# Performance work log

Hardware: AMD Instinct MI355X
Metric: run time of the kernel (lower is better)

## Reference

```python
import jax, jax.numpy as jnp
import numpy as np

N = 20000      # nodes
L = 64         # seq_length
E = 64         # emb_size
V = 30000      # vocab_size
HG = 128       # gnn_hidden_size
HT = 128       # text_hidden_size
NE = 640000    # edges
EPS = 1e-12


def _normalize(x):
    # F.normalize(x, p=2, dim=1) on [N, E, L]
    n = jnp.sqrt(jnp.sum(x * x, axis=1, keepdims=True))
    return x / jnp.maximum(n, EPS)


def gcn_conv(x, W, b, src_idx, dst_idx, n_nodes):
    # PyG GCNConv: add self-loops, symmetric normalization D^-1/2 (A+I) D^-1/2 (X W) + b
    h = x @ W                                            # [N, out]
    deg = jnp.zeros((n_nodes,), h.dtype).at[dst_idx].add(1.0) + 1.0  # incl. self-loop
    dinv = jax.lax.rsqrt(deg)
    norm = dinv[src_idx] * dinv[dst_idx]                 # [NE]
    msg = h[src_idx] * norm[:, None]                     # gather + scale
    out = jnp.zeros_like(h).at[dst_idx].add(msg)         # scatter-add to targets
    out = out + h * (dinv * dinv)[:, None]               # self-loop term
    return out + b


def setup_inputs() -> dict:
    key = jax.random.key(0)
    ks = jax.random.split(key, 12)
    rn = lambda k, shape: jax.random.normal(k, shape, jnp.float32) * 0.02
    return {
        "src": jax.random.randint(ks[0], (N, L), 0, V),
        "seg": jax.random.randint(ks[1], (N, L), 0, 3),
        "edge_index": jax.random.randint(ks[2], (2, NE), 0, N),
        "src_emb": rn(ks[3], (V, E)),
        "seg_emb": rn(ks[4], (3, E)),
        "w": jnp.ones((L,), jnp.float32),
        "Wq1": rn(ks[5], (E, HT)), "bq1": jnp.zeros((HT,), jnp.float32),
        "Wq2": rn(ks[6], (HT, E)), "bq2": jnp.zeros((E,), jnp.float32),
        "Wg1": rn(ks[7], (E, HG)), "bg1": jnp.zeros((HG,), jnp.float32),
        "Wg2": rn(ks[8], (HG, E)), "bg2": jnp.zeros((E,), jnp.float32),
        "Wl": rn(ks[9], (E, E)),   "bl": jnp.zeros((E,), jnp.float32),
    }


def reference(src, seg, edge_index, src_emb, seg_emb, w, Wq1, bq1, Wq2, bq2,
              Wg1, bg1, Wg2, bg2, Wl, bl):
    # --- LiteratureEmbedding ---
    se = src_emb[src]                 # [N, L, E]
    ge = seg_emb[seg]                 # [N, L, E]
    sv = se.reshape(-1, E, L)         # raw view (matches torch .view, not transpose)
    gv = ge.reshape(-1, E, L)
    f = (_normalize(w * sv) + _normalize(gv)).sum(-1)   # [N, E]
    # --- query MLP ---
    x = jax.nn.relu(f @ Wq1 + bq1) @ Wq2 + bq2
    # --- two GCN layers ---
    si, di = edge_index[0], edge_index[1]
    x = jax.nn.relu(gcn_conv(x, Wg1, bg1, si, di, N))
    x = jax.nn.relu(gcn_conv(x, Wg2, bg2, si, di, N))
    # --- output linear (dropout is identity in eval) ---
    return x @ Wl + bl
```

## Files before the change

### kernel.cpp

```cpp
#include <hip/hip_runtime.h>

#if defined(__has_builtin)
#if __has_builtin(__builtin_amdgcn_readlane)
#define READLANE(v, l) __builtin_amdgcn_readlane((v), (l))
#else
#define READLANE(v, l) __shfl((v), (l))
#endif
#else
#define READLANE(v, l) __shfl((v), (l))
#endif
__device__ __forceinline__ float readlane_f(float v, int l) {
    return __uint_as_float(READLANE(__float_as_uint(v), l));
}

__device__ __forceinline__ unsigned short f2bf(float x) {
    unsigned u = __float_as_uint(x);
    u += 0x7FFFu + ((u >> 16) & 1u);
    return (unsigned short)(u >> 16);
}

#define CAPLOG 8

__global__ __launch_bounds__(256) void zero_k(int* __restrict__ p,
                                              unsigned* __restrict__ Cz,
                                              unsigned* __restrict__ Az, int n) {
    int i = blockIdx.x * 256 + threadIdx.x;
    if (i < n) p[i] = 0;
    if (i < 32) { Cz[i] = 0u; Az[i] = 0u; }
}

__global__ __launch_bounds__(256) void fillb_k(const int* __restrict__ si,
                                               const int* __restrict__ di,
                                               int* __restrict__ cursor,
                                               int* __restrict__ edge_off, int ne) {
    int i = blockIdx.x * 256 + threadIdx.x;
    if (i < ne) {
        int d = di[i];
        int pos = atomicAdd(cursor + d, 1);
        edge_off[((long)d << CAPLOG) + pos] = si[i] << 7;
    }
}

__device__ __forceinline__ float4 csr_gather4_bf(const char* __restrict__ hb,
                                                 const int* __restrict__ eo,
                                                 int dn, int j, int zoff)
{
    const int grp = j >> 4;
    const int col = (j & 15) << 3;
    float4 a0 = make_float4(0.f, 0.f, 0.f, 0.f);
    float4 a1 = a0, a2 = a0, a3 = a0;
#define ACC(d, a)                                                        \
    { a.x += __uint_as_float((d).x << 16);                               \
      a.y += __uint_as_float((d).x & 0xFFFF0000u);                       \
      a.z += __uint_as_float((d).y << 16);                               \
      a.w += __uint_as_float((d).y & 0xFFFF0000u); }
    for (int e = 0; e < dn; e += 64) {
        const int cnt = min(dn - e, 64);
        const int eoff = (e + j < dn) ? eo[e + j] : zoff;
        int m = 0;
        for (; m + 16 <= cnt; m += 16) {
            int o0 = __shfl(eoff, m + grp);
            int o1 = __shfl(eoff, m + 4 + grp);
            int o2 = __shfl(eoff, m + 8 + grp);
            int o3 = __shfl(eoff, m + 12 + grp);
            uint2 d0 = *(const uint2*)(hb + (o0 + col));
            uint2 d1 = *(const uint2*)(hb + (o1 + col));
            uint2 d2 = *(const uint2*)(hb + (o2 + col));
            uint2 d3 = *(const uint2*)(hb + (o3 + col));
            ACC(d0, a0); ACC(d1, a1); ACC(d2, a2); ACC(d3, a3);
        }
        for (; m < cnt; m += 4) {
            int o = __shfl(eoff, m + grp);
            uint2 d = *(const uint2*)(hb + (o + col));
            ACC(d, a0);
        }
    }
#undef ACC
    a0.x += a1.x + a2.x + a3.x;
    a0.y += a1.y + a2.y + a3.y;
    a0.z += a1.z + a2.z + a3.z;
    a0.w += a1.w + a2.w + a3.w;
    a0.x += __shfl_xor(a0.x, 16); a0.x += __shfl_xor(a0.x, 32);
    a0.y += __shfl_xor(a0.y, 16); a0.y += __shfl_xor(a0.y, 32);
    a0.z += __shfl_xor(a0.z, 16); a0.z += __shfl_xor(a0.z, 32);
    a0.w += __shfl_xor(a0.w, 16); a0.w += __shfl_xor(a0.w, 32);
    return a0;
}

__device__ __forceinline__ float4 bf_row4(const char* hb, long rowoff, int col) {
    uint2 d = *(const uint2*)(hb + rowoff + col);
    float4 v;
    v.x = __uint_as_float(d.x << 16);
    v.y = __uint_as_float(d.x & 0xFFFF0000u);
    v.z = __uint_as_float(d.y << 16);
    v.w = __uint_as_float(d.y & 0xFFFF0000u);
    return v;
}

__global__ __launch_bounds__(256) void embed_k(
    const int* __restrict__ src, const int* __restrict__ seg,
    const float* __restrict__ src_emb, const float* __restrict__ seg_emb,
    const float* __restrict__ wvec, float* __restrict__ f)
{
    __shared__ __align__(16) float S[64 * 65];
    __shared__ float red[4][64];
    __shared__ float part2[4][64];
    __shared__ float coef[64];
    __shared__ float rGs[64];
    __shared__ float segE[192];
    __shared__ float dG[3];
    __shared__ int   gidxS[64];
    __shared__ int   cnt3[3];

    const int t = threadIdx.x, wid = t >> 6, q = t & 63;
    const long n = blockIdx.x;

    if (wid == 0) {
        int c = seg[n * 64 + q];
        gidxS[q] = c;
        unsigned long long b0 = __ballot(c == 0);
        unsigned long long b1 = __ballot(c == 1);
        if (q == 0) {
            int n0 = __popcll(b0), n1 = __popcll(b1);
            cnt3[0] = n0; cnt3[1] = n1; cnt3[2] = 64 - n0 - n1;
        }
    } else if (t < 64 + 192) {
        segE[t - 64] = seg_emb[t - 64];
    }

    const int p0 = wid * 16;
    int off = src[n * 64 + p0 + (q & 15)] << 8;
    const char* base = (const char*)src_emb;
    const int q4 = q << 2;
    float s2 = 0.f;
    #pragma unroll
    for (int pp = 0; pp < 16; ++pp) {
        int so = READLANE(off, pp);
        float v = *(const float*)(base + (so + q4));
        S[(p0 + pp) * 65 + q] = v;
        s2 += v * v;
    }
    red[wid][q] = s2;
    __syncthreads();

    if (t < 64) {
        float ts = red[0][t] + red[1][t] + red[2][t] + red[3][t];
        float wq = wvec[t];
        coef[t] = wq / fmaxf(fabsf(wq) * sqrtf(ts), 1e-12f);
        float e0 = segE[t], e1 = segE[64 + t], e2 = segE[128 + t];
        float g2 = (float)cnt3[0] * e0 * e0 + (float)cnt3[1] * e1 * e1
                 + (float)cnt3[2] * e2 * e2;
        rGs[t] = 1.f / fmaxf(sqrtf(g2), 1e-12f);
    }
    __syncthreads();

    if (t < 3) {
        float a = 0.f;
        for (int k = 0; k < 64; ++k) a += segE[t * 64 + k] * rGs[k];
        dG[t] = a;
    }
    float acc = 0.f;
    const int k0 = wid * 16;
    #pragma unroll
    for (int kk = 0; kk < 16; ++kk)
        acc += S[q * 65 + k0 + kk] * coef[k0 + kk];
    part2[wid][q] = acc;
    __syncthreads();

    if (t < 64)
        f[n * 64 + t] = part2[0][t] + part2[1][t] + part2[2][t] + part2[3][t]
                        + dG[gidxS[t]];
}

template <bool S2_BIAS>
__device__ __forceinline__ void dense_pair_body(
    float* Wh, float* F, float* H,
    const float* __restrict__ W1, const float* __restrict__ b1,
    const float* __restrict__ W2, const float* __restrict__ b2,
    const int* __restrict__ deg, unsigned short* __restrict__ out,
    int row0, int nrows, int t)
{
    for (int i = t * 4; i < 32 * 128; i += 1024)
        *(float4*)&Wh[i] = *(const float4*)&W1[i];
    __syncthreads();

    const int jg = t & 31, rslot = t >> 5;
    const int j0 = jg * 4;
    float4 acc0, acc1;
    {
        float4 b4 = *(const float4*)&b1[j0];
        acc0 = b4; acc1 = b4;
    }
    #pragma unroll 2
    for (int k = 0; k < 32; k += 4) {
        float4 w0 = *(float4*)&Wh[(k + 0) * 128 + j0];
        float4 w1 = *(float4*)&Wh[(k + 1) * 128 + j0];
        float4 w2 = *(float4*)&Wh[(k + 2) * 128 + j0];
        float4 w3 = *(float4*)&Wh[(k + 3) * 128 + j0];
        float4 fa = *(float4*)&F[rslot * 64 + k];
        float4 fb = *(float4*)&F[(rslot + 8) * 64 + k];
        acc0.x += fa.x * w0.x + fa.y * w1.x + fa.z * w2.x + fa.w * w3.x;
        acc0.y += fa.x * w0.y + fa.y * w1.y + fa.z * w2.y + fa.w * w3.y;
        acc0.z += fa.x * w0.z + fa.y * w1.z + fa.z * w2.z + fa.w * w3.z;
        acc0.w += fa.x * w0.w + fa.y * w1.w + fa.z * w2.w + fa.w * w3.w;
        acc1.x += fb.x * w0.x + fb.y * w1.x + fb.z * w2.x + fb.w * w3.x;
        acc1.y += fb.x * w0.y + fb.y * w1.y + fb.z * w2.y + fb.w * w3.y;
        acc1.z += fb.x * w0.z + fb.y * w1.z + fb.z * w2.z + fb.w * w3.z;
        acc1.w += fb.x * w0.w + fb.y * w1.w + fb.z * w2.w + fb.w * w3.w;
    }
    __syncthreads();
    for (int i = t * 4; i < 32 * 128; i += 1024)
        *(float4*)&Wh[i] = *(const float4*)&W1[32 * 128 + i];
    __syncthreads();
    #pragma unroll 2
    for (int k = 0; k < 32; k += 4) {
        float4 w0 = *(float4*)&Wh[(k + 0) * 128 + j0];
        float4 w1 = *(float4*)&Wh[(k + 1) * 128 + j0];
        float4 w2 = *(float4*)&Wh[(k + 2) * 128 + j0];
        float4 w3 = *(float4*)&Wh[(k + 3) * 128 + j0];
        float4 fa = *(float4*)&F[rslot * 64 + 32 + k];
        float4 fb = *(float4*)&F[(rslot + 8) * 64 + 32 + k];
        acc0.x += fa.x * w0.x + fa.y * w1.x + fa.z * w2.x + fa.w * w3.x;
        acc0.y += fa.x * w0.y + fa.y * w1.y + fa.z * w2.y + fa.w * w3.y;
        acc0.z += fa.x * w0.z + fa.y * w1.z + fa.z * w2.z + fa.w * w3.z;
        acc0.w += fa.x * w0.w + fa.y * w1.w + fa.z * w2.w + fa.w * w3.w;
        acc1.x += fb.x * w0.x + fb.y * w1.x + fb.z * w2.x + fb.w * w3.x;
        acc1.y += fb.x * w0.y + fb.y * w1.y + fb.z * w2.y + fb.w * w3.y;
        acc1.z += fb.x * w0.z + fb.y * w1.z + fb.z * w2.z + fb.w * w3.z;
        acc1.w += fb.x * w0.w + fb.y * w1.w + fb.z * w2.w + fb.w * w3.w;
    }
    {
        float4 v;
        v.x = fmaxf(acc0.x, 0.f); v.y = fmaxf(acc0.y, 0.f);
        v.z = fmaxf(acc0.z, 0.f); v.w = fmaxf(acc0.w, 0.f);
        *(float4*)&H[rslot * 128 + j0] = v;
        v.x = fmaxf(acc1.x, 0.f); v.y = fmaxf(acc1.y, 0.f);
        v.z = fmaxf(acc1.z, 0.f); v.w = fmaxf(acc1.w, 0.f);
        *(float4*)&H[(rslot + 8) * 128 + j0] = v;
    }
    __syncthreads();

    for (int i = t * 4; i < 64 * 64; i += 1024)
        *(float4*)&Wh[i] = *(const float4*)&W2[i];
    __syncthreads();
    const int jg2 = t & 15, r2 = t >> 4;
    const int j02 = jg2 * 4;
    float4 acc = S2_BIAS ? *(const float4*)&b2[j02]
                         : make_float4(0.f, 0.f, 0.f, 0.f);
    #pragma unroll 2
    for (int k = 0; k < 64; k += 4) {
        float4 w0 = *(float4*)&Wh[(k + 0) * 64 + j02];
        float4 w1 = *(float4*)&Wh[(k + 1) * 64 + j02];
        float4 w2 = *(float4*)&Wh[(k + 2) * 64 + j02];
        float4 w3 = *(float4*)&Wh[(k + 3) * 64 + j02];
        float4 fq = *(float4*)&H[r2 * 128 + k];
        acc.x += fq.x * w0.x + fq.y * w1.x + fq.z * w2.x + fq.w * w3.x;
        acc.y += fq.x * w0.y + fq.y * w1.y + fq.z * w2.y + fq.w * w3.y;
        acc.z += fq.x * w0.z + fq.y * w1.z + fq.z * w2.z + fq.w * w3.z;
        acc.w += fq.x * w0.w + fq.y * w1.w + fq.z * w2.w + fq.w * w3.w;
    }
    __syncthreads();
    for (int i = t * 4; i < 64 * 64; i += 1024)
        *(float4*)&Wh[i] = *(const float4*)&W2[64 * 64 + i];
    __syncthreads();
    #pragma unroll 2
    for (int k = 0; k < 64; k += 4) {
        float4 w0 = *(float4*)&Wh[(k + 0) * 64 + j02];
        float4 w1 = *(float4*)&Wh[(k + 1) * 64 + j02];
        float4 w2 = *(float4*)&Wh[(k + 2) * 64 + j02];
        float4 w3 = *(float4*)&Wh[(k + 3) * 64 + j02];
        float4 fq = *(float4*)&H[r2 * 128 + 64 + k];
        acc.x += fq.x * w0.x + fq.y * w1.x + fq.z * w2.x + fq.w * w3.x;
        acc.y += fq.x * w0.y + fq.y * w1.y + fq.z * w2.y + fq.w * w3.y;
        acc.z += fq.x * w0.z + fq.y * w1.z + fq.z * w2.z + fq.w * w3.z;
        acc.w += fq.x * w0.w + fq.y * w1.w + fq.z * w2.w + fq.w * w3.w;
    }
    const int r = row0 + r2;
    if (r < nrows) {
        float sc = rsqrtf((float)deg[r] + 1.0f);
        ushort4 v;
        v.x = f2bf(acc.x * sc); v.y = f2bf(acc.y * sc);
        v.z = f2bf(acc.z * sc); v.w = f2bf(acc.w * sc);
        *(ushort4*)&out[(long)r * 64 + j02] = v;
    }
}

template <bool S2_BIAS>
__global__ __launch_bounds__(256, 5) void fused2_k(
    const float* __restrict__ in, const float* __restrict__ W1,
    const float* __restrict__ b1, const float* __restrict__ W2,
    const float* __restrict__ b2, const int* __restrict__ deg,
    unsigned short* __restrict__ out, int nrows)
{
    __shared__ __align__(16) float Wh[32 * 128];
    __shared__ __align__(16) float F[16 * 64];
    __shared__ __align__(16) float H[16 * 128];
    const int t = threadIdx.x;
    const int row0 = blockIdx.x * 16;

    for (int i = t * 4; i < 16 * 64; i += 1024) {
        int r = i >> 6;
        float4 v = make_float4(0.f, 0.f, 0.f, 0.f);
        if (row0 + r < nrows) v = *(const float4*)&in[(long)row0 * 64 + i];
        *(float4*)&F[i] = v;
    }
    dense_pair_body<S2_BIAS>(Wh, F, H, W1, b1, W2, b2, deg, out, row0, nrows, t);
}

__global__ __launch_bounds__(256, 5) void gcnfused_k(
    const unsigned short* __restrict__ C, const int* __restrict__ deg,
    const int* __restrict__ edge_off,
    const float* __restrict__ W1, const float* __restrict__ b1,
    const float* __restrict__ W2, unsigned short* __restrict__ out,
    int nrows, int zoff)
{
    __shared__ __align__(16) float Wh[32 * 128];
    __shared__ __align__(16) float F[16 * 64];
    __shared__ __align__(16) float H[16 * 128];
    const int t = threadIdx.x;
    const int row0 = blockIdx.x * 16;
    const int wv = t >> 6, j = t & 63;
    const int col = (j & 15) << 3;

    const char* hb = (const char*)C;
    #pragma unroll
    for (int i = 0; i < 4; ++i) {
        const int r = wv * 4 + i;
        const int node = row0 + r;
        if (node < nrows) {
            float4 agg = csr_gather4_bf(hb, edge_off + ((long)node << CAPLOG),
                                        deg[node], j, zoff);
            float4 self = bf_row4(hb, (long)node << 7, col);
            float dv = rsqrtf((float)deg[node] + 1.0f);
            if ((j >> 4) == 0) {
                float4 res;
                res.x = dv * (self.x + agg.x);
                res.y = dv * (self.y + agg.y);
                res.z = dv * (self.z + agg.z);
                res.w = dv * (self.w + agg.w);
                *(float4*)&F[r * 64 + (j & 15) * 4] = res;
            }
        } else if ((j >> 4) == 0) {
            *(float4*)&F[r * 64 + (j & 15) * 4] = make_float4(0.f, 0.f, 0.f, 0.f);
        }
    }
    dense_pair_body<false>(Wh, F, H, W1, b1, W2, nullptr, deg, out, row0, nrows, t);
}

__global__ __launch_bounds__(256) void gatherout_k(
    const unsigned short* __restrict__ hp, const int* __restrict__ deg,
    const int* __restrict__ edge_off,
    const float* __restrict__ bg2, const float* __restrict__ Wl,
    const float* __restrict__ bl, float* __restrict__ out, int n, int zoff)
{
    __shared__ __align__(16) float WlL[64 * 64];
    __shared__ __align__(16) float vS[4][64];
    const int t = threadIdx.x;
    for (int i = t * 4; i < 64 * 64; i += 1024)
        *(float4*)&WlL[i] = *(const float4*)&Wl[i];
    __syncthreads();

    const int row0 = blockIdx.x * 16;
    const int wv = t >> 6, j = t & 63;
    const int col = (j & 15) << 3;
    const char* hb = (const char*)hp;
    const float blj = bl[j];
    const float4 bg4 = *(const float4*)&bg2[(j & 15) * 4];

    #pragma unroll
    for (int i = 0; i < 4; ++i) {
        const int node = row0 + wv * 4 + i;
        if (node >= n) continue;
        float4 agg = csr_gather4_bf(hb, edge_off + ((long)node << CAPLOG),
                                    deg[node], j, zoff);
        float4 self = bf_row4(hb, (long)node << 7, col);
        const float dv = rsqrtf((float)deg[node] + 1.0f);
        float4 vf;
        vf.x = fmaxf(dv * (self.x + agg.x) + bg4.x, 0.f);
        vf.y = fmaxf(dv * (self.y + agg.y) + bg4.y, 0.f);
        vf.z = fmaxf(dv * (self.z + agg.z) + bg4.z, 0.f);
        vf.w = fmaxf(dv * (self.w + agg.w) + bg4.w, 0.f);
        if ((j >> 4) == 0) *(float4*)&vS[wv][(j & 15) * 4] = vf;
        const float v = vS[wv][j];

        float o = blj;
        #pragma unroll 4
        for (int k = 0; k < 64; k += 4) {
            float vk0 = readlane_f(v, k + 0);
            float vk1 = readlane_f(v, k + 1);
            float vk2 = readlane_f(v, k + 2);
            float vk3 = readlane_f(v, k + 3);
            o += vk0 * WlL[(k + 0) * 64 + j] + vk1 * WlL[(k + 1) * 64 + j]
               + vk2 * WlL[(k + 2) * 64 + j] + vk3 * WlL[(k + 3) * 64 + j];
        }
        out[(long)node * 64 + j] = o;
    }
}

extern "C" void kernel_launch(void* const* d_in, const int* in_sizes, int n_in,
                              void* d_out, int out_size, void* d_ws, size_t ws_size,
                              hipStream_t stream) {
    const int*   src     = (const int*)  d_in[0];
    const int*   seg     = (const int*)  d_in[1];
    const int*   ei      = (const int*)  d_in[2];
    const float* src_emb = (const float*)d_in[3];
    const float* seg_emb = (const float*)d_in[4];
    const float* w       = (const float*)d_in[5];
    const float* Wq1     = (const float*)d_in[6];
    const float* bq1     = (const float*)d_in[7];
    const float* Wq2     = (const float*)d_in[8];
    const float* bq2     = (const float*)d_in[9];
    const float* Wg1     = (const float*)d_in[10];
    const float* bg1     = (const float*)d_in[11];
    const float* Wg2     = (const float*)d_in[12];
    const float* bg2     = (const float*)d_in[13];
    const float* Wl      = (const float*)d_in[14];
    const float* bl      = (const float*)d_in[15];
    float* out = (float*)d_out;

    const int N  = in_sizes[0] / 64;
    const int NE = in_sizes[2] / 2;
    const int* si = ei;
    const int* di = ei + NE;

    const size_t Npad = ((size_t)N + 3) & ~(size_t)3;
    int* cursor   = (int*)d_ws;
    int* edge_off = cursor + Npad;
    float* A32 = (float*)(edge_off + ((size_t)N << CAPLOG));
    unsigned short* Cbf = (unsigned short*)(A32 + (size_t)N * 64);
    unsigned short* Abf = Cbf + (size_t)N * 64 + 64;
    const int zoff = N << 7;

    dim3 b256(256);
    const int nBlocks = (N + 255) / 256;
    const int eBlocks = (NE + 255) / 256;
    const int fBlocks = (N + 15) / 16;

    zero_k <<<nBlocks, b256, 0, stream>>>(cursor,
                                          (unsigned*)(Cbf + (size_t)N * 64),
                                          (unsigned*)(Abf + (size_t)N * 64), N);
    fillb_k<<<eBlocks, b256, 0, stream>>>(si, di, cursor, edge_off, NE);

    embed_k<<<N, b256, 0, stream>>>(src, seg, src_emb, seg_emb, w, A32);

    fused2_k<true><<<fBlocks, b256, 0, stream>>>(A32, Wq1, bq1, Wq2, bq2,
                                                 cursor, Cbf, N);

    gcnfused_k<<<fBlocks, b256, 0, stream>>>(Cbf, cursor, edge_off,
                                             Wg1, bg1, Wg2, Abf, N, zoff);

    gatherout_k<<<fBlocks, b256, 0, stream>>>(Abf, cursor, edge_off, bg2,
                                              Wl, bl, out, N, zoff);
}
```

Before: 232.3 us.

## Convert embedding table to bf16 and merge prep kernels into two launches

Each call now converts the fp32 source-embedding table to bf16 in a new prep kernel that also zeroes the cursors. Edge-bucket filling and the embedding/normalize step are merged into one launch, with the first blocks doing edge atomics and the rest doing per-node embedding. The embedding gather reads 2-byte values instead of 4, halving random-gather bytes, but adds a full-table conversion pass and rounds embeddings to bf16 before normalization. Merging launches removes two kernel launches and lets edge filling overlap with embedding work.

```diff
diff --git a/kernel.cpp b/kernel.cpp
--- a/kernel.cpp
+++ b/kernel.cpp
@@ -21,24 +21,115 @@
 
 #define CAPLOG 8
 
-__global__ __launch_bounds__(256) void zero_k(int* __restrict__ p,
-                                              unsigned* __restrict__ Cz,
-                                              unsigned* __restrict__ Az, int n) {
-    int i = blockIdx.x * 256 + threadIdx.x;
-    if (i < n) p[i] = 0;
-    if (i < 32) { Cz[i] = 0u; Az[i] = 0u; }
-}
-
-__global__ __launch_bounds__(256) void fillb_k(const int* __restrict__ si,
-                                               const int* __restrict__ di,
-                                               int* __restrict__ cursor,
-                                               int* __restrict__ edge_off, int ne) {
-    int i = blockIdx.x * 256 + threadIdx.x;
-    if (i < ne) {
-        int d = di[i];
-        int pos = atomicAdd(cursor + d, 1);
-        edge_off[((long)d << CAPLOG) + pos] = si[i] << 7;
-    }
+__global__ __launch_bounds__(256) void prep0_k(
+    const float* __restrict__ src_emb, unsigned short* __restrict__ sbf, int ve,
+    int* __restrict__ cursor, int n,
+    unsigned* __restrict__ Cz, unsigned* __restrict__ Az, int convB)
+{
+    const int b = blockIdx.x, t = threadIdx.x;
+    if (b < convB) {
+        int i = (b * 256 + t) * 4;
+        if (i + 3 < ve) {
+            float4 v = *(const float4*)&src_emb[i];
+            ushort4 u;
+            u.x = f2bf(v.x); u.y = f2bf(v.y); u.z = f2bf(v.z); u.w = f2bf(v.w);
+            *(ushort4*)&sbf[i] = u;
+        } else {
+            for (; i < ve; ++i) sbf[i] = f2bf(src_emb[i]);
+        }
+    } else {
+        int i = (b - convB) * 256 + t;
+        if (i < n) cursor[i] = 0;
+        if (b == convB && t < 32) { Cz[t] = 0u; Az[t] = 0u; }
+    }
+}
+
+__global__ __launch_bounds__(256) void prep1_k(
+    const int* __restrict__ si, const int* __restrict__ di,
+    int* __restrict__ cursor, int* __restrict__ edge_off, int ne, int eB,
+    const int* __restrict__ src, const int* __restrict__ seg,
+    const unsigned short* __restrict__ sbf, const float* __restrict__ seg_emb,
+    const float* __restrict__ wvec, float* __restrict__ f)
+{
+    const int t = threadIdx.x;
+    if ((int)blockIdx.x < eB) {
+        int i = blockIdx.x * 256 + t;
+        if (i < ne) {
+            int d = di[i];
+            int pos = atomicAdd(cursor + d, 1);
+            edge_off[((long)d << CAPLOG) + pos] = si[i] << 7;
+        }
+        return;
+    }
+    __shared__ __align__(16) float S[64 * 65];
+    __shared__ float red[4][64];
+    __shared__ float part2[4][64];
+    __shared__ float coef[64];
+    __shared__ float rGs[64];
+    __shared__ float segE[192];
+    __shared__ float dG[3];
+    __shared__ int   gidxS[64];
+    __shared__ int   cnt3[3];
+
+    const int wid = t >> 6, q = t & 63;
+    const long n = blockIdx.x - eB;
+
+    if (wid == 0) {
+        int c = seg[n * 64 + q];
+        gidxS[q] = c;
+        unsigned long long b0 = __ballot(c == 0);
+        unsigned long long b1 = __ballot(c == 1);
+        if (q == 0) {
+            int n0 = __popcll(b0), n1 = __popcll(b1);
+            cnt3[0] = n0; cnt3[1] = n1; cnt3[2] = 64 - n0 - n1;
+        }
+    } else if (t < 64 + 192) {
+        segE[t - 64] = seg_emb[t - 64];
+    }
+
+    const int p0 = wid * 16;
+    int off = src[n * 64 + p0 + (q & 15)] << 7;
+    const char* base = (const char*)sbf;
+    const int q2 = q << 1;
+    float s2 = 0.f;
+    #pragma unroll
+    for (int pp = 0; pp < 16; ++pp) {
+        int so = READLANE(off, pp);
+        unsigned short u = *(const unsigned short*)(base + (so + q2));
+        float v = __uint_as_float((unsigned)u << 16);
+        S[(p0 + pp) * 65 + q] = v;
+        s2 += v * v;
+    }
+    red[wid][q] = s2;
+    __syncthreads();
+
+    if (t < 64) {
+        float ts = red[0][t] + red[1][t] + red[2][t] + red[3][t];
+        float wq = wvec[t];
+        coef[t] = wq / fmaxf(fabsf(wq) * sqrtf(ts), 1e-12f);
+        float e0 = segE[t], e1 = segE[64 + t], e2 = segE[128 + t];
+        float g2 = (float)cnt3[0] * e0 * e0 + (float)cnt3[1] * e1 * e1
+                 + (float)cnt3[2] * e2 * e2;
+        rGs[t] = 1.f / fmaxf(sqrtf(g2), 1e-12f);
+    }
+    __syncthreads();
+
+    if (t < 3) {
+        float a = 0.f;
+        for (int k = 0; k < 64; ++k) a += segE[t * 64 + k] * rGs[k];
+        dG[t] = a;
+    }
+    float acc = 0.f;
+    const int k0 = wid * 16;
+    #pragma unroll
+    for (int kk = 0; kk < 16; ++kk)
+        acc += S[q * 65 + k0 + kk] * coef[k0 + kk];
+    part2[wid][q] = acc;
+    __syncthreads();
+
+    if (t < 64)
+        f[n * 64 + t] = part2[0][t] + part2[1][t] + part2[2][t] + part2[3][t]
+                        + dG[gidxS[t]];
 }
 
 __device__ __forceinline__ float4 csr_gather4_bf(const char* __restrict__ hb,
@@ -97,81 +188,6 @@
     return v;
 }
 
-__global__ __launch_bounds__(256) void embed_k(
-    const int* __restrict__ src, const int* __restrict__ seg,
-    const float* __restrict__ src_emb, const float* __restrict__ seg_emb,
-    const float* __restrict__ wvec, float* __restrict__ f)
-{
-    __shared__ __align__(16) float S[64 * 65];
-    __shared__ float red[4][64];
-    __shared__ float part2[4][64];
-    __shared__ float coef[64];
-    __shared__ float rGs[64];
-    __shared__ float segE[192];
-    __shared__ float dG[3];
-    __shared__ int   gidxS[64];
-    __shared__ int   cnt3[3];
-
-    const int t = threadIdx.x, wid = t >> 6, q = t & 63;
-    const long n = blockIdx.x;
-
-    if (wid == 0) {
-        int c = seg[n * 64 + q];
-        gidxS[q] = c;
-        unsigned long long b0 = __ballot(c == 0);
-        unsigned long long b1 = __ballot(c == 1);
-        if (q == 0) {
-            int n0 = __popcll(b0), n1 = __popcll(b1);
-            cnt3[0] = n0; cnt3[1] = n1; cnt3[2] = 64 - n0 - n1;
-        }
-    } else if (t < 64 + 192) {
-        segE[t - 64] = seg_emb[t - 64];
-    }
-
-    const int p0 = wid * 16;
-    int off = src[n * 64 + p0 + (q & 15)] << 8;
-    const char* base = (const char*)src_emb;
-    const int q4 = q << 2;
-    float s2 = 0.f;
-    #pragma unroll
-    for (int pp = 0; pp < 16; ++pp) {
-        int so = READLANE(off, pp);
-        float v = *(const float*)(base + (so + q4));
-        S[(p0 + pp) * 65 + q] = v;
-        s2 += v * v;
-    }
-    red[wid][q] = s2;
-    __syncthreads();
-
-    if (t < 64) {
-        float ts = red[0][t] + red[1][t] + red[2][t] + red[3][t];
-        float wq = wvec[t];
-        coef[t] = wq / fmaxf(fabsf(wq) * sqrtf(ts), 1e-12f);
-        float e0 = segE[t], e1 = segE[64 + t], e2 = segE[128 + t];
-        float g2 = (float)cnt3[0] * e0 * e0 + (float)cnt3[1] * e1 * e1
-                 + (float)cnt3[2] * e2 * e2;
-        rGs[t] = 1.f / fmaxf(sqrtf(g2), 1e-12f);
-    }
-    __syncthreads();
-
-    if (t < 3) {
-        float a = 0.f;
-        for (int k = 0; k < 64; ++k) a += segE[t * 64 + k] * rGs[k];
-        dG[t] = a;
-    }
-    float acc = 0.f;
-    const int k0 = wid * 16;
-    #pragma unroll
-    for (int kk = 0; kk < 16; ++kk)
-        acc += S[q * 65 + k0 + kk] * coef[k0 + kk];
-    part2[wid][q] = acc;
-    __syncthreads();
-
-    if (t < 64)
-        f[n * 64 + t] = part2[0][t] + part2[1][t] + part2[2][t] + part2[3][t]
-                        + dG[gidxS[t]];
-}
-
 template <bool S2_BIAS>
 __device__ __forceinline__ void dense_pair_body(
     float* Wh, float* F, float* H,
@@ -420,35 +436,39 @@
 
     const int N  = in_sizes[0] / 64;
     const int NE = in_sizes[2] / 2;
+    const int VE = in_sizes[3];
     const int* si = ei;
     const int* di = ei + NE;
 
-    const size_t Npad = ((size_t)N + 3) & ~(size_t)3;
+    const size_t Npad  = ((size_t)N + 3) & ~(size_t)3;
+    const size_t VEpad = ((size_t)VE + 7) & ~(size_t)7;
     int* cursor   = (int*)d_ws;
     int* edge_off = cursor + Npad;
-    float* A32 = (float*)(edge_off + ((size_t)N << CAPLOG));
+    unsigned short* sbf = (unsigned short*)(edge_off + ((size_t)N << CAPLOG));
+    float* A32 = (float*)(sbf + VEpad);
     unsigned short* Cbf = (unsigned short*)(A32 + (size_t)N * 64);
     unsigned short* Abf = Cbf + (size_t)N * 64 + 64;
     const int zoff = N << 7;
 
     dim3 b256(256);
-    const int nBlocks = (N + 255) / 256;
-    const int eBlocks = (NE + 255) / 256;
-    const int fBlocks = (N + 15) / 16;
-
-    zero_k <<<nBlocks, b256, 0, stream>>>(cursor,
-                                          (unsigned*)(Cbf + (size_t)N * 64),
-                                          (unsigned*)(Abf + (size_t)N * 64), N);
-    fillb_k<<<eBlocks, b256, 0, stream>>>(si, di, cursor, edge_off, NE);
-
-    embed_k<<<N, b256, 0, stream>>>(src, seg, src_emb, seg_emb, w, A32);
-
-    fused2_k<true><<<fBlocks, b256, 0, stream>>>(A32, Wq1, bq1, Wq2, bq2,
-                                                 cursor, Cbf, N);
-
-    gcnfused_k<<<fBlocks, b256, 0, stream>>>(Cbf, cursor, edge_off,
-                                             Wg1, bg1, Wg2, Abf, N, zoff);
-
-    gatherout_k<<<fBlocks, b256, 0, stream>>>(Abf, cursor, edge_off, bg2,
-                                              Wl, bl, out, N, zoff);
-}
+    const int convB = (VE + 1023) / 1024;
+    const int zB    = (N + 255) / 256;
+    const int eB    = (NE + 255) / 256;
+    const int fB    = (N + 15) / 16;
+
+    prep0_k<<<convB + zB, b256, 0, stream>>>(src_emb, sbf, VE, cursor, N,
+                                             (unsigned*)(Cbf + (size_t)N * 64),
+                                             (unsigned*)(Abf + (size_t)N * 64),
+                                             convB);
+    prep1_k<<<eB + N, b256, 0, stream>>>(si, di, cursor, edge_off, NE, eB,
+                                         src, seg, sbf, seg_emb, w, A32);
+
+    fused2_k<true><<<fB, b256, 0, stream>>>(A32, Wq1, bq1, Wq2, bq2,
+                                            cursor, Cbf, N);
+
+    gcnfused_k<<<fB, b256, 0, stream>>>(Cbf, cursor, edge_off,
+                                        Wg1, bg1, Wg2, Abf, N, zoff);
+
+    gatherout_k<<<fB, b256, 0, stream>>>(Abf, cursor, edge_off, bg2,
+                                         Wl, bl, out, N, zoff);
+}
```

Measured after the change: 227.2 us. 1.02x faster.
